# Performance work log

Measured on AMD Instinct MI355X. Metric: run time of the kernel, lower is better.

## Reference

```python
import jax, jax.numpy as jnp
import numpy as np

B, T, D_MODEL, H, HD = 2, 2048, 2048, 16, 128
TOTAL = H * HD


def setup_inputs() -> dict:
    key = jax.random.key(0)
    ks = jax.random.split(key, 7)
    s = 1.0 / np.sqrt(D_MODEL)
    x = jax.random.normal(ks[0], (B, T, D_MODEL), dtype=jnp.float32)
    cos = jax.random.uniform(ks[1], (T, HD), dtype=jnp.float32)
    sin = jax.random.uniform(ks[2], (T, HD), dtype=jnp.float32)
    Wq = jax.random.normal(ks[3], (D_MODEL, TOTAL), dtype=jnp.float32) * s
    Wk = jax.random.normal(ks[4], (D_MODEL, TOTAL), dtype=jnp.float32) * s
    Wv = jax.random.normal(ks[5], (D_MODEL, TOTAL), dtype=jnp.float32) * s
    Wo = jax.random.normal(ks[6], (TOTAL, D_MODEL), dtype=jnp.float32) * s
    return {"x": x, "cos": cos, "sin": sin, "Wq": Wq, "Wk": Wk, "Wv": Wv, "Wo": Wo}


def rotate_half(x):
    x1, x2 = jnp.split(x, 2, axis=-1)
    return jnp.concatenate([-x2, x1], axis=-1)


def reference(x, cos, sin, Wq, Wk, Wv, Wo):
    b, t, _ = x.shape
    # QKV projections -> [B, H, T, HD]
    q = (x @ Wq).reshape(b, t, H, HD).transpose(0, 2, 1, 3)
    k = (x @ Wk).reshape(b, t, H, HD).transpose(0, 2, 1, 3)
    v = (x @ Wv).reshape(b, t, H, HD).transpose(0, 2, 1, 3)
    # RoPE (cos/sin broadcast [T,HD] -> [B,H,T,HD])
    q = q * cos + rotate_half(q) * sin
    k = k * cos + rotate_half(k) * sin
    # causal SDPA (kv_cache=None branch), eval mode -> no dropout
    scale = HD ** -0.5
    scores = jnp.einsum('bhqd,bhkd->bhqk', q, k) * scale
    causal = jnp.tril(jnp.ones((t, t), dtype=bool))
    scores = jnp.where(causal, scores, jnp.asarray(-1e9, scores.dtype))
    attn = jax.nn.softmax(scores, axis=-1)
    out = jnp.einsum('bhqk,bhkd->bhqd', attn, v)
    out = out.transpose(0, 2, 1, 3).reshape(b, t, TOTAL)
    return out @ Wo, k, v
```

## Files before the change

### kernel.cpp

```cpp
#include <hip/hip_runtime.h>


typedef __bf16 bf16;
typedef __attribute__((ext_vector_type(8))) __bf16 bf16x8;
typedef __attribute__((ext_vector_type(4))) __bf16 bf16x4;
typedef __attribute__((ext_vector_type(4))) float f32x4;

__device__ __forceinline__ void gload_lds16(const void* g, void* l) {
  __builtin_amdgcn_global_load_lds((const __attribute__((address_space(1))) void*)g,
                                   (__attribute__((address_space(3))) void*)l, 16, 0, 0);
}

__global__ __launch_bounds__(256) void k_convert(const float* __restrict__ in,
                                                 bf16* __restrict__ out, int n4) {
  int i = blockIdx.x * 256 + threadIdx.x;
  if (i >= n4) return;
  float4 v = ((const float4*)in)[i];
  bf16x4 o;
  o.x = (bf16)v.x; o.y = (bf16)v.y; o.z = (bf16)v.z; o.w = (bf16)v.w;
  ((bf16x4*)out)[i] = o;
}

__global__ __launch_bounds__(256) void k_transpose_w(
    const float* __restrict__ W0, const float* __restrict__ W1,
    const float* __restrict__ W2, const float* __restrict__ W3,
    bf16* __restrict__ T0, bf16* __restrict__ T1,
    bf16* __restrict__ T2, bf16* __restrict__ T3) {
  __shared__ float tile[32][33];
  const float* W; bf16* To;
  switch (blockIdx.z) {
    case 0: W = W0; To = T0; break;
    case 1: W = W1; To = T1; break;
    case 2: W = W2; To = T2; break;
    default: W = W3; To = T3; break;
  }
  int n0 = blockIdx.x * 32, k0 = blockIdx.y * 32;
  int tx = threadIdx.x, ty = threadIdx.y;
#pragma unroll
  for (int j = 0; j < 4; ++j)
    tile[ty + 8 * j][tx] = W[(size_t)(k0 + ty + 8 * j) * 2048 + n0 + tx];
  __syncthreads();
#pragma unroll
  for (int j = 0; j < 4; ++j)
    To[(size_t)(n0 + ty + 8 * j) * 2048 + k0 + tx] = (bf16)tile[tx][ty + 8 * j];
}

template <int MODE>
__global__ __launch_bounds__(256) void k_gemm(
    const bf16* __restrict__ A, const bf16* __restrict__ B0,
    const bf16* __restrict__ B1, const bf16* __restrict__ B2,
    bf16* __restrict__ o0, bf16* __restrict__ o1, bf16* __restrict__ o2,
    float* __restrict__ outf) {
  __shared__ __align__(16) bf16 Al[128 * 64];
  __shared__ __align__(16) bf16 Bl[128 * 64];
  const bf16* Bt; bf16* outb = nullptr;
  if (MODE == 0) {
    switch (blockIdx.z) {
      case 0: Bt = B0; outb = o0; break;
      case 1: Bt = B1; outb = o1; break;
      default: Bt = B2; outb = o2; break;
    }
  } else {
    Bt = B0;
  }
  int t = threadIdx.x;
  int wv = t >> 6, lane = t & 63, lr = lane & 15, lg = lane >> 4;
  int wr = wv >> 1, wc = wv & 1;
  int row0 = blockIdx.x * 128, col0 = blockIdx.y * 128;
  f32x4 acc[4][4] = {};
  for (int kt = 0; kt < 32; ++kt) {
    int k0 = kt * 64;
#pragma unroll
    for (int it = 0; it < 4; ++it) {
      int ci = it * 256 + t;
      int r = ci >> 3, c8 = (ci & 7) * 8;
      int base = __builtin_amdgcn_readfirstlane(it * 256 + (t & ~63));
      gload_lds16(A + (size_t)(row0 + r) * 2048 + k0 + c8, Al + (size_t)base * 8);
      gload_lds16(Bt + (size_t)(col0 + r) * 2048 + k0 + c8, Bl + (size_t)base * 8);
    }
    __syncthreads();
#pragma unroll
    for (int kk = 0; kk < 2; ++kk) {
      bf16x8 af[4], bfr[4];
#pragma unroll
      for (int mf = 0; mf < 4; ++mf)
        af[mf] = *(const bf16x8*)(Al + (wr * 64 + mf * 16 + lr) * 64 + kk * 32 + lg * 8);
#pragma unroll
      for (int nf = 0; nf < 4; ++nf)
        bfr[nf] = *(const bf16x8*)(Bl + (wc * 64 + nf * 16 + lr) * 64 + kk * 32 + lg * 8);
#pragma unroll
      for (int mf = 0; mf < 4; ++mf)
#pragma unroll
        for (int nf = 0; nf < 4; ++nf)
          acc[mf][nf] = __builtin_amdgcn_mfma_f32_16x16x32_bf16(af[mf], bfr[nf], acc[mf][nf], 0, 0, 0);
    }
    __syncthreads();
  }
#pragma unroll
  for (int mf = 0; mf < 4; ++mf)
#pragma unroll
    for (int nf = 0; nf < 4; ++nf)
#pragma unroll
      for (int r = 0; r < 4; ++r) {
        int row = row0 + wr * 64 + mf * 16 + lg * 4 + r;
        int col = col0 + wc * 64 + nf * 16 + lr;
        float v = acc[mf][nf][r];
        if (MODE == 0) {
          int b = row >> 11, tt = row & 2047, h = col >> 7, d = col & 127;
          outb[(size_t)((b * 16 + h) * 2048 + tt) * 128 + d] = (bf16)v;
        } else {
          outf[(size_t)row * 2048 + col] = v;
        }
      }
}

__global__ __launch_bounds__(256) void k_rope(
    bf16* __restrict__ q, bf16* __restrict__ k, const bf16* __restrict__ v,
    const float* __restrict__ cosb, const float* __restrict__ sinb,
    float* __restrict__ kout, float* __restrict__ vout) {
  int tid = blockIdx.x * 256 + threadIdx.x;
  int d = tid & 63;
  int row = tid >> 6;
  int t = row & 2047;
  size_t base = (size_t)row * 128;
  float c1 = cosb[t * 128 + d], c2 = cosb[t * 128 + 64 + d];
  float s1 = sinb[t * 128 + d], s2 = sinb[t * 128 + 64 + d];
  float qlo = (float)q[base + d], qhi = (float)q[base + 64 + d];
  float klo = (float)k[base + d], khi = (float)k[base + 64 + d];
  float ql = qlo * c1 - qhi * s1, qh = qhi * c2 + qlo * s2;
  float kl = klo * c1 - khi * s1, kh = khi * c2 + klo * s2;
  q[base + d] = (bf16)ql; q[base + 64 + d] = (bf16)qh;
  k[base + d] = (bf16)kl; k[base + 64 + d] = (bf16)kh;
  kout[base + d] = kl; kout[base + 64 + d] = kh;
  vout[base + d] = (float)v[base + d];
  vout[base + 64 + d] = (float)v[base + 64 + d];
}

__global__ __launch_bounds__(256) void k_vt(const bf16* __restrict__ v,
                                            bf16* __restrict__ vt) {
  __shared__ bf16 tile[32][33];
  int bh = blockIdx.z;
  int t0 = blockIdx.x * 32, d0 = blockIdx.y * 32;
  int tx = threadIdx.x, ty = threadIdx.y;
  const bf16* vb = v + (size_t)bh * 2048 * 128;
  bf16* vtb = vt + (size_t)bh * 128 * 2048;
#pragma unroll
  for (int j = 0; j < 4; ++j)
    tile[ty + 8 * j][tx] = vb[(size_t)(t0 + ty + 8 * j) * 128 + d0 + tx];
  __syncthreads();
#pragma unroll
  for (int j = 0; j < 4; ++j)
    vtb[(size_t)(d0 + ty + 8 * j) * 2048 + t0 + tx] = tile[tx][ty + 8 * j];
}

__global__ __launch_bounds__(256) void k_attn(
    const bf16* __restrict__ Q, const bf16* __restrict__ Kr,
    const bf16* __restrict__ Vt, bf16* __restrict__ O) {
  __shared__ __align__(16) bf16 Vtl[128][40];
  __shared__ __align__(16) bf16 Pl[4][16][32];
  int t = threadIdx.x, wv = t >> 6, lane = t & 63, lr = lane & 15, lg = lane >> 4;
  int qb = blockIdx.x, bh = blockIdx.y;
  int qbase = qb * 64, wq0 = qbase + wv * 16;
  const bf16* Qb = Q + (size_t)bh * 2048 * 128;
  const bf16* Kb = Kr + (size_t)bh * 2048 * 128;
  const bf16* Vb = Vt + (size_t)bh * 128 * 2048;
  bf16x8 qf[4];
#pragma unroll
  for (int df = 0; df < 4; ++df)
    qf[df] = *(const bf16x8*)(Qb + (size_t)(wq0 + lr) * 128 + df * 32 + lg * 8);
  f32x4 od[8] = {};
  float m_run[4], l_run[4];
#pragma unroll
  for (int r = 0; r < 4; ++r) { m_run[r] = -1e30f; l_run[r] = 0.f; }
  const float scale = 0.08838834764831845f;
  int nkt = 2 * qb + 2;
  for (int kt = 0; kt < nkt; ++kt) {
    int kv0 = kt * 32;
    bf16x8 vreg[2];
#pragma unroll
    for (int it = 0; it < 2; ++it) {
      int d = it * 64 + (t >> 2), c8 = (t & 3) * 8;
      vreg[it] = *(const bf16x8*)(Vb + (size_t)d * 2048 + kv0 + c8);
    }
    bool active = (kv0 <= wq0 + 15);
    if (active) {
      f32x4 s[2] = {};
#pragma unroll
      for (int c = 0; c < 2; ++c)
#pragma unroll
        for (int df = 0; df < 4; ++df) {
          bf16x8 kf = *(const bf16x8*)(Kb + (size_t)(kv0 + c * 16 + lr) * 128 + df * 32 + lg * 8);
          s[c] = __builtin_amdgcn_mfma_f32_16x16x32_bf16(qf[df], kf, s[c], 0, 0, 0);
        }
      float p[2][4], corr[4];
#pragma unroll
      for (int r = 0; r < 4; ++r) {
        int qrow = wq0 + lg * 4 + r;
        float s0 = s[0][r] * scale, s1 = s[1][r] * scale;
        if (kv0 + lr > qrow) s0 = -1e30f;
        if (kv0 + 16 + lr > qrow) s1 = -1e30f;
        float mx = fmaxf(s0, s1);
        mx = fmaxf(mx, __shfl_xor(mx, 1));
        mx = fmaxf(mx, __shfl_xor(mx, 2));
        mx = fmaxf(mx, __shfl_xor(mx, 4));
        mx = fmaxf(mx, __shfl_xor(mx, 8));
        float mnew = fmaxf(m_run[r], mx);
        float cr = __expf(m_run[r] - mnew);
        float p0 = __expf(s0 - mnew), p1 = __expf(s1 - mnew);
        float rs = p0 + p1;
        rs += __shfl_xor(rs, 1); rs += __shfl_xor(rs, 2);
        rs += __shfl_xor(rs, 4); rs += __shfl_xor(rs, 8);
        l_run[r] = l_run[r] * cr + rs;
        m_run[r] = mnew;
        corr[r] = cr;
        p[0][r] = p0; p[1][r] = p1;
      }
#pragma unroll
      for (int db = 0; db < 8; ++db)
#pragma unroll
        for (int r = 0; r < 4; ++r) od[db][r] *= corr[r];
#pragma unroll
      for (int c = 0; c < 2; ++c)
#pragma unroll
        for (int r = 0; r < 4; ++r)
          Pl[wv][lg * 4 + r][c * 16 + lr] = (bf16)p[c][r];
    }
#pragma unroll
    for (int it = 0; it < 2; ++it) {
      int d = it * 64 + (t >> 2), c8 = (t & 3) * 8;
      *(bf16x8*)(&Vtl[d][c8]) = vreg[it];
    }
    __syncthreads();
    if (active) {
      bf16x8 pa = *(const bf16x8*)(&Pl[wv][lr][lg * 8]);
#pragma unroll
      for (int db = 0; db < 8; ++db) {
        bf16x8 vb = *(const bf16x8*)(&Vtl[db * 16 + lr][lg * 8]);
        od[db] = __builtin_amdgcn_mfma_f32_16x16x32_bf16(pa, vb, od[db], 0, 0, 0);
      }
    }
    __syncthreads();
  }
  int b = bh >> 4, h = bh & 15;
#pragma unroll
  for (int db = 0; db < 8; ++db)
#pragma unroll
    for (int r = 0; r < 4; ++r) {
      int q = wq0 + lg * 4 + r;
      float v = od[db][r] / l_run[r];
      O[(size_t)(b * 2048 + q) * 2048 + h * 128 + db * 16 + lr] = (bf16)v;
    }
}

extern "C" void kernel_launch(void* const* d_in, const int* in_sizes, int n_in,
                              void* d_out, int out_size, void* d_ws, size_t ws_size,
                              hipStream_t stream) {
  const float* x    = (const float*)d_in[0];
  const float* cosb = (const float*)d_in[1];
  const float* sinb = (const float*)d_in[2];
  const float* Wq   = (const float*)d_in[3];
  const float* Wk   = (const float*)d_in[4];
  const float* Wv   = (const float*)d_in[5];
  const float* Wo   = (const float*)d_in[6];
  float* out  = (float*)d_out;
  float* kout = out + (size_t)8388608;
  float* vout = out + (size_t)16777216;

  char* ws = (char*)d_ws;
  bf16* xb  = (bf16*)(ws);
  bf16* WqT = (bf16*)(ws + (size_t)16777216);
  bf16* WkT = (bf16*)(ws + (size_t)25165824);
  bf16* WvT = (bf16*)(ws + (size_t)33554432);
  bf16* WoT = (bf16*)(ws + (size_t)41943040);
  bf16* qb  = (bf16*)(ws + (size_t)50331648);
  bf16* kb  = (bf16*)(ws + (size_t)67108864);
  bf16* vb  = (bf16*)(ws + (size_t)83886080);
  bf16* vt  = (bf16*)(ws + (size_t)100663296);
  bf16* ao  = xb;

  k_convert<<<8192, 256, 0, stream>>>(x, xb, 2097152);
  k_transpose_w<<<dim3(64, 64, 4), dim3(32, 8), 0, stream>>>(Wq, Wk, Wv, Wo,
                                                             WqT, WkT, WvT, WoT);
  k_gemm<0><<<dim3(32, 16, 3), 256, 0, stream>>>(xb, WqT, WkT, WvT,
                                                 qb, kb, vb, nullptr);
  k_rope<<<16384, 256, 0, stream>>>(qb, kb, vb, cosb, sinb, kout, vout);
  k_vt<<<dim3(64, 4, 32), dim3(32, 8), 0, stream>>>(vb, vt);
  k_attn<<<dim3(32, 32), 256, 0, stream>>>(qb, kb, vt, ao);
  k_gemm<1><<<dim3(32, 16, 1), 256, 0, stream>>>(ao, WoT, nullptr, nullptr,
                                                 nullptr, nullptr, nullptr, out);
}
```

Measured before the change: 750.3 us.

## Restructure attention kernel: 128-row q tiles, 64-key steps, direct V loads

Each attention block now covers 128 query rows, with each wave owning two 16-row fragments, and steps over 64 keys at a time, so every loaded K and V fragment feeds two MFMA chains. V is read directly from global memory instead of being staged through shared memory, which removes both block-wide barriers. P goes through a per-wave XOR-swizzled LDS buffer guarded only by a waitcnt. Blocks are launched in reverse order so the longest causal rows start first. The costs are higher register pressure (launch bounds set to 2 blocks per SIMD), half as many blocks, and uncoalesced-ish global V reads that rely on cache.

```diff
diff --git a/kernel.cpp b/kernel.cpp
--- a/kernel.cpp
+++ b/kernel.cpp
@@ -153,103 +153,119 @@
     vtb[(size_t)(d0 + ty + 8 * j) * 2048 + t0 + tx] = tile[tx][ty + 8 * j];
 }
 
-__global__ __launch_bounds__(256) void k_attn(
+__global__ __launch_bounds__(256, 2) void k_attn(
     const bf16* __restrict__ Q, const bf16* __restrict__ Kr,
     const bf16* __restrict__ Vt, bf16* __restrict__ O) {
-  __shared__ __align__(16) bf16 Vtl[128][40];
-  __shared__ __align__(16) bf16 Pl[4][16][32];
+  __shared__ __align__(16) bf16 Pl[4][2][16][64];
   int t = threadIdx.x, wv = t >> 6, lane = t & 63, lr = lane & 15, lg = lane >> 4;
-  int qb = blockIdx.x, bh = blockIdx.y;
-  int qbase = qb * 64, wq0 = qbase + wv * 16;
+  int qb = (int)gridDim.x - 1 - (int)blockIdx.x;
+  int bh = blockIdx.y;
+  int qbase = qb * 128;
   const bf16* Qb = Q + (size_t)bh * 2048 * 128;
   const bf16* Kb = Kr + (size_t)bh * 2048 * 128;
   const bf16* Vb = Vt + (size_t)bh * 128 * 2048;
-  bf16x8 qf[4];
-#pragma unroll
-  for (int df = 0; df < 4; ++df)
-    qf[df] = *(const bf16x8*)(Qb + (size_t)(wq0 + lr) * 128 + df * 32 + lg * 8);
-  f32x4 od[8] = {};
-  float m_run[4], l_run[4];
-#pragma unroll
-  for (int r = 0; r < 4; ++r) { m_run[r] = -1e30f; l_run[r] = 0.f; }
+  int wq[2] = {qbase + wv * 16, qbase + 64 + wv * 16};
+  bf16x8 qf[2][4];
+#pragma unroll
+  for (int mf = 0; mf < 2; ++mf)
+#pragma unroll
+    for (int df = 0; df < 4; ++df)
+      qf[mf][df] = *(const bf16x8*)(Qb + (size_t)(wq[mf] + lr) * 128 + df * 32 + lg * 8);
+  f32x4 od[2][8] = {};
+  float m_run[2][4], l_run[2][4];
+#pragma unroll
+  for (int mf = 0; mf < 2; ++mf)
+#pragma unroll
+    for (int r = 0; r < 4; ++r) { m_run[mf][r] = -1e30f; l_run[mf][r] = 0.f; }
   const float scale = 0.08838834764831845f;
   int nkt = 2 * qb + 2;
   for (int kt = 0; kt < nkt; ++kt) {
-    int kv0 = kt * 32;
-    bf16x8 vreg[2];
-#pragma unroll
-    for (int it = 0; it < 2; ++it) {
-      int d = it * 64 + (t >> 2), c8 = (t & 3) * 8;
-      vreg[it] = *(const bf16x8*)(Vb + (size_t)d * 2048 + kv0 + c8);
-    }
-    bool active = (kv0 <= wq0 + 15);
-    if (active) {
-      f32x4 s[2] = {};
-#pragma unroll
-      for (int c = 0; c < 2; ++c)
-#pragma unroll
-        for (int df = 0; df < 4; ++df) {
-          bf16x8 kf = *(const bf16x8*)(Kb + (size_t)(kv0 + c * 16 + lr) * 128 + df * 32 + lg * 8);
-          s[c] = __builtin_amdgcn_mfma_f32_16x16x32_bf16(qf[df], kf, s[c], 0, 0, 0);
+    int kv0 = kt * 64;
+    f32x4 s[2][4] = {};
+#pragma unroll
+    for (int c = 0; c < 4; ++c) {
+      bf16x8 kf[4];
+#pragma unroll
+      for (int df = 0; df < 4; ++df)
+        kf[df] = *(const bf16x8*)(Kb + (size_t)(kv0 + c * 16 + lr) * 128 + df * 32 + lg * 8);
+#pragma unroll
+      for (int mf = 0; mf < 2; ++mf)
+#pragma unroll
+        for (int df = 0; df < 4; ++df)
+          s[mf][c] = __builtin_amdgcn_mfma_f32_16x16x32_bf16(qf[mf][df], kf[df], s[mf][c], 0, 0, 0);
+    }
+    bool act0 = (kv0 <= wq[0] + 15);
+#pragma unroll
+    for (int mf = 0; mf < 2; ++mf) {
+      if (mf == 0 && !act0) continue;
+      float corr[4];
+#pragma unroll
+      for (int r = 0; r < 4; ++r) {
+        int qrow = wq[mf] + lg * 4 + r;
+        float sv[4];
+#pragma unroll
+        for (int c = 0; c < 4; ++c) {
+          sv[c] = s[mf][c][r] * scale;
+          if (kv0 + c * 16 + lr > qrow) sv[c] = -1e30f;
         }
-      float p[2][4], corr[4];
-#pragma unroll
-      for (int r = 0; r < 4; ++r) {
-        int qrow = wq0 + lg * 4 + r;
-        float s0 = s[0][r] * scale, s1 = s[1][r] * scale;
-        if (kv0 + lr > qrow) s0 = -1e30f;
-        if (kv0 + 16 + lr > qrow) s1 = -1e30f;
-        float mx = fmaxf(s0, s1);
+        float mx = fmaxf(fmaxf(sv[0], sv[1]), fmaxf(sv[2], sv[3]));
         mx = fmaxf(mx, __shfl_xor(mx, 1));
         mx = fmaxf(mx, __shfl_xor(mx, 2));
         mx = fmaxf(mx, __shfl_xor(mx, 4));
         mx = fmaxf(mx, __shfl_xor(mx, 8));
-        float mnew = fmaxf(m_run[r], mx);
-        float cr = __expf(m_run[r] - mnew);
-        float p0 = __expf(s0 - mnew), p1 = __expf(s1 - mnew);
-        float rs = p0 + p1;
+        float mnew = fmaxf(m_run[mf][r], mx);
+        float cr = __expf(m_run[mf][r] - mnew);
+        float pv0 = __expf(sv[0] - mnew), pv1 = __expf(sv[1] - mnew);
+        float pv2 = __expf(sv[2] - mnew), pv3 = __expf(sv[3] - mnew);
+        float rs = pv0 + pv1 + pv2 + pv3;
         rs += __shfl_xor(rs, 1); rs += __shfl_xor(rs, 2);
         rs += __shfl_xor(rs, 4); rs += __shfl_xor(rs, 8);
-        l_run[r] = l_run[r] * cr + rs;
-        m_run[r] = mnew;
+        l_run[mf][r] = l_run[mf][r] * cr + rs;
+        m_run[mf][r] = mnew;
         corr[r] = cr;
-        p[0][r] = p0; p[1][r] = p1;
+        int row = lg * 4 + r, sw = (row & 7) * 8;
+        Pl[wv][mf][row][(0 * 16 + lr) ^ sw] = (bf16)pv0;
+        Pl[wv][mf][row][(1 * 16 + lr) ^ sw] = (bf16)pv1;
+        Pl[wv][mf][row][(2 * 16 + lr) ^ sw] = (bf16)pv2;
+        Pl[wv][mf][row][(3 * 16 + lr) ^ sw] = (bf16)pv3;
       }
 #pragma unroll
       for (int db = 0; db < 8; ++db)
 #pragma unroll
-        for (int r = 0; r < 4; ++r) od[db][r] *= corr[r];
-#pragma unroll
-      for (int c = 0; c < 2; ++c)
-#pragma unroll
-        for (int r = 0; r < 4; ++r)
-          Pl[wv][lg * 4 + r][c * 16 + lr] = (bf16)p[c][r];
-    }
-#pragma unroll
-    for (int it = 0; it < 2; ++it) {
-      int d = it * 64 + (t >> 2), c8 = (t & 3) * 8;
-      *(bf16x8*)(&Vtl[d][c8]) = vreg[it];
-    }
-    __syncthreads();
-    if (active) {
-      bf16x8 pa = *(const bf16x8*)(&Pl[wv][lr][lg * 8]);
+        for (int r = 0; r < 4; ++r) od[mf][db][r] *= corr[r];
+    }
+    __builtin_amdgcn_sched_barrier(0);
+    __builtin_amdgcn_s_waitcnt(0xc07f);
+    __builtin_amdgcn_sched_barrier(0);
+    bf16x8 pa[2][2];
+#pragma unroll
+    for (int mf = 0; mf < 2; ++mf) {
+      if (mf == 0 && !act0) continue;
+#pragma unroll
+      for (int kk = 0; kk < 2; ++kk)
+        pa[mf][kk] = *(const bf16x8*)(&Pl[wv][mf][lr][(kk * 32 + lg * 8) ^ ((lr & 7) * 8)]);
+    }
+#pragma unroll
+    for (int kk = 0; kk < 2; ++kk)
 #pragma unroll
       for (int db = 0; db < 8; ++db) {
-        bf16x8 vb = *(const bf16x8*)(&Vtl[db * 16 + lr][lg * 8]);
-        od[db] = __builtin_amdgcn_mfma_f32_16x16x32_bf16(pa, vb, od[db], 0, 0, 0);
+        bf16x8 vf = *(const bf16x8*)(Vb + (size_t)(db * 16 + lr) * 2048 + kv0 + kk * 32 + lg * 8);
+        if (act0)
+          od[0][db] = __builtin_amdgcn_mfma_f32_16x16x32_bf16(pa[0][kk], vf, od[0][db], 0, 0, 0);
+        od[1][db] = __builtin_amdgcn_mfma_f32_16x16x32_bf16(pa[1][kk], vf, od[1][db], 0, 0, 0);
       }
-    }
-    __syncthreads();
   }
   int b = bh >> 4, h = bh & 15;
 #pragma unroll
-  for (int db = 0; db < 8; ++db)
-#pragma unroll
-    for (int r = 0; r < 4; ++r) {
-      int q = wq0 + lg * 4 + r;
-      float v = od[db][r] / l_run[r];
-      O[(size_t)(b * 2048 + q) * 2048 + h * 128 + db * 16 + lr] = (bf16)v;
-    }
+  for (int mf = 0; mf < 2; ++mf)
+#pragma unroll
+    for (int db = 0; db < 8; ++db)
+#pragma unroll
+      for (int r = 0; r < 4; ++r) {
+        int q = wq[mf] + lg * 4 + r;
+        float v = od[mf][db][r] / l_run[mf][r];
+        O[(size_t)(b * 2048 + q) * 2048 + h * 128 + db * 16 + lr] = (bf16)v;
+      }
 }
 
 extern "C" void kernel_launch(void* const* d_in, const int* in_sizes, int n_in,
@@ -285,7 +301,7 @@
                                                  qb, kb, vb, nullptr);
   k_rope<<<16384, 256, 0, stream>>>(qb, kb, vb, cosb, sinb, kout, vout);
   k_vt<<<dim3(64, 4, 32), dim3(32, 8), 0, stream>>>(vb, vt);
-  k_attn<<<dim3(32, 32), 256, 0, stream>>>(qb, kb, vt, ao);
+  k_attn<<<dim3(16, 32), 256, 0, stream>>>(qb, kb, vt, ao);
   k_gemm<1><<<dim3(32, 16, 1), 256, 0, stream>>>(ao, WoT, nullptr, nullptr,
                                                  nullptr, nullptr, nullptr, out);
 }
```

After: 674.5 us. 1.11x faster.
